# Kernel optimization log

Hardware: AMD Instinct MI355X
Metric: run time of the kernel (lower is better)

The kernel has to match this reference:

```python
import jax, jax.numpy as jnp
import numpy as np

NUM_HEADS = 16


def setup_inputs() -> dict:
    key = jax.random.key(0)
    ks = jax.random.split(key, 5)
    B, S, D = 2, 2048, 1024
    scale = 0.02
    return {
        "x": jax.random.normal(ks[0], (B, S, D), dtype=jnp.float32),
        "Wq": jax.random.normal(ks[1], (D, D), dtype=jnp.float32) * scale,
        "Wk": jax.random.normal(ks[2], (D, D), dtype=jnp.float32) * scale,
        "Wv": jax.random.normal(ks[3], (D, D), dtype=jnp.float32) * scale,
        "Wo": jax.random.normal(ks[4], (D, D), dtype=jnp.float32) * scale,
        "bo": jnp.zeros((D,), dtype=jnp.float32),
    }


def reference(x, Wq, Wk, Wv, Wo, bo):
    B, S, D = x.shape
    H = NUM_HEADS
    Dh = D // H
    # project and split heads -> [B, H, S, Dh]
    q = (x @ Wq).reshape(B, S, H, Dh).transpose(0, 2, 1, 3)
    k = (x @ Wk).reshape(B, S, H, Dh).transpose(0, 2, 1, 3)
    v = (x @ Wv).reshape(B, S, H, Dh).transpose(0, 2, 1, 3)
    # full causal attention scores [B, H, S, S]
    scores = jnp.einsum("bhqd,bhkd->bhqk", q, k)
    causal_mask = jnp.triu(jnp.ones((S, S), dtype=bool), k=1)
    scores = jnp.where(causal_mask, -jnp.inf, scores)
    attn = jax.nn.softmax(scores / jnp.sqrt(jnp.float32(Dh)), axis=-1)
    ctx = jnp.einsum("bhqk,bhkd->bhqd", attn, v)
    ctx = ctx.transpose(0, 2, 1, 3).reshape(B, S, D)
    return ctx @ Wo + bo
```

## Files before the change

kernel.cpp:

```cpp
#include <hip/hip_runtime.h>
#include <hip/hip_bf16.h>
#include <math.h>

typedef __bf16 bf16_t;
typedef bf16_t bf16x4 __attribute__((ext_vector_type(4)));
typedef bf16_t bf16x8 __attribute__((ext_vector_type(8)));
typedef float f32x4 __attribute__((ext_vector_type(4)));

#define MFMA16(a, b, c) __builtin_amdgcn_mfma_f32_16x16x32_bf16(a, b, c, 0, 0, 0)
#define NEG_BIG (-1e30f)
#define QSCALE 0.18033688f

#define GLL16(gp, lp)                                                          \
    __builtin_amdgcn_global_load_lds(                                          \
        (const __attribute__((address_space(1))) unsigned int*)(gp),           \
        (__attribute__((address_space(3))) unsigned int*)(lp), 16, 0, 0)


__global__ __launch_bounds__(256) void prep(const float* __restrict__ x,
                                            const float* __restrict__ Wq,
                                            const float* __restrict__ Wk,
                                            const float* __restrict__ Wv,
                                            const float* __restrict__ Wo,
                                            bf16_t* __restrict__ Xb,
                                            bf16_t* __restrict__ WTqkv,
                                            bf16_t* __restrict__ WoT) {
    __shared__ float tile[32][33];
    const int z = blockIdx.z;
    const int tx = threadIdx.x, ty = threadIdx.y;
    if (z == 4) {
        int i0 = (((blockIdx.y * 32 + blockIdx.x) * 256) + ty * 32 + tx) * 4;
        for (int j = 0; j < 4; j++) {
            int i = i0 + j * 1048576;
            float4 v = *(const float4*)(x + i);
            Xb[i + 0] = (bf16_t)v.x;
            Xb[i + 1] = (bf16_t)v.y;
            Xb[i + 2] = (bf16_t)v.z;
            Xb[i + 3] = (bf16_t)v.w;
        }
    } else {
        const float* W = (z == 0) ? Wq : (z == 1) ? Wk : (z == 2) ? Wv : Wo;
        bf16_t* WT = (z < 3) ? (WTqkv + (size_t)z * 1048576) : WoT;
        int bx = blockIdx.x * 32, by = blockIdx.y * 32;
        for (int i = 0; i < 32; i += 8)
            tile[ty + i][tx] = W[(size_t)(by + ty + i) * 1024 + bx + tx];
        __syncthreads();
        for (int i = 0; i < 32; i += 8)
            WT[(size_t)(bx + ty + i) * 1024 + by + tx] = (bf16_t)tile[tx][ty + i];
    }
}

__global__ __launch_bounds__(256) void gemm_qkv(const bf16_t* __restrict__ X,
                                                const bf16_t* __restrict__ WT,
                                                bf16_t* __restrict__ Qd,
                                                bf16_t* __restrict__ Kd,
                                                bf16_t* __restrict__ Vd) {
    __shared__ bf16_t AsmF[128 * 64];
    __shared__ bf16_t BsmF[128 * 64];
    const int which = blockIdx.z;
    const bf16_t* Wt = WT + (size_t)which * 1024 * 1024;
    const int bm = blockIdx.y * 128;
    const int bn = blockIdx.x * 128;
    const int tid = threadIdx.x;
    const int wave = tid >> 6, lane = tid & 63;
    const int wm = (wave >> 1) * 64, wn = (wave & 1) * 64;
    const int col = lane & 15, quad = lane >> 4;
    const int cswz = col & 7;
    const int lr8 = lane >> 3;
    const int jg = (lane & 7) ^ lr8;

    const int srow = wave * 32 + lr8;
    const bf16_t* gA = X  + (size_t)(bm + srow) * 1024 + jg * 8;
    const bf16_t* gB = Wt + (size_t)(bn + srow) * 1024 + jg * 8;
    bf16_t* lA = AsmF + wave * 2048;
    bf16_t* lB = BsmF + wave * 2048;

    f32x4 acc[4][4] = {};

    for (int k0 = 0; k0 < 1024; k0 += 64) {
        for (int j = 0; j < 4; j++) {
            GLL16(gA + (size_t)j * 8192 + k0, lA + j * 512);
            GLL16(gB + (size_t)j * 8192 + k0, lB + j * 512);
        }
        __syncthreads();
        for (int ks = 0; ks < 2; ks++) {
            bf16x8 af[4], bfr[4];
            for (int mi = 0; mi < 4; mi++)
                af[mi] = *(const bf16x8*)&AsmF[(wm + mi * 16 + col) * 64 +
                                               (((ks << 2) + quad) ^ cswz) * 8];
            for (int ni = 0; ni < 4; ni++)
                bfr[ni] = *(const bf16x8*)&BsmF[(wn + ni * 16 + col) * 64 +
                                                (((ks << 2) + quad) ^ cswz) * 8];
            if (which != 2) {
                for (int mi = 0; mi < 4; mi++)
                    for (int ni = 0; ni < 4; ni++)
                        acc[mi][ni] = MFMA16(af[mi], bfr[ni], acc[mi][ni]);
            } else {
                for (int mi = 0; mi < 4; mi++)
                    for (int ni = 0; ni < 4; ni++)
                        acc[mi][ni] = MFMA16(bfr[ni], af[mi], acc[mi][ni]);
            }
        }
        __syncthreads();
    }

    if (which != 2) {
        const float sc = (which == 0) ? QSCALE : 1.0f;
        for (int mi = 0; mi < 4; mi++) {
            for (int ni = 0; ni < 4; ni++) {
                int mbase = bm + wm + mi * 16 + quad * 4;
                int n = bn + wn + ni * 16 + col;
                int h = n >> 6, dh = n & 63;
                for (int r = 0; r < 4; r++) {
                    int m = mbase + r;
                    int b = m >> 11, s = m & 2047;
                    size_t bh = (size_t)b * 16 + h;
                    bf16_t val = (bf16_t)(acc[mi][ni][r] * sc);
                    if (which == 0) Qd[(bh * 2048 + s) * 64 + dh] = val;
                    else            Kd[(bh * 2048 + s) * 64 + dh] = val;
                }
            }
        }
    } else {
        for (int mi = 0; mi < 4; mi++) {
            for (int ni = 0; ni < 4; ni++) {
                int nbase = bn + wn + ni * 16 + quad * 4;
                int m = bm + wm + mi * 16 + col;
                int b = m >> 11, s = m & 2047;
                for (int r = 0; r < 4; r++) {
                    int n = nbase + r;
                    int h = n >> 6, dh = n & 63;
                    size_t bh = (size_t)b * 16 + h;
                    Vd[(bh * 64 + dh) * 2048 + s] = (bf16_t)acc[mi][ni][r];
                }
            }
        }
    }
}

#define PSD 72
__global__ __launch_bounds__(256) void attn(const bf16_t* __restrict__ Q,
                                            const bf16_t* __restrict__ K,
                                            const bf16_t* __restrict__ VT,
                                            bf16_t* __restrict__ CTX) {
    __shared__ bf16_t KsF[2 * 64 * 64];
    __shared__ bf16_t VsF[2 * 64 * 64];
    __shared__ bf16_t Ps[4][16][PSD];

    const int bidx = blockIdx.x;
    const int bh = bidx & 31;
    const int pr = bidx >> 5;
    const int qt0 = pr, qt1 = 31 - pr;
    const int tid = threadIdx.x;
    const int wave = tid >> 6, lane = tid & 63;
    const int col = lane & 15, quad = lane >> 4;
    const int cswz = col & 7;
    const int lr8 = lane >> 3;
    const int jg = (lane & 7) ^ lr8;

    const bf16_t* Qb = Q + (size_t)bh * 2048 * 64;
    const bf16_t* Kb = K + (size_t)bh * 2048 * 64;
    const bf16_t* Vb = VT + (size_t)bh * 64 * 2048;

    const int strow = wave * 16 + lr8;
    const bf16_t* gK = Kb + (size_t)strow * 64 + jg * 8;
    const bf16_t* gV = Vb + (size_t)strow * 2048 + jg * 8;

    const int b_ = bh >> 4, h_ = bh & 15;

    bf16x8 ones;
    for (int i = 0; i < 8; i++) ones[i] = (bf16_t)1.0f;

    auto stage = [&](int k0, int bsel) {
        bf16_t* lK = KsF + bsel * 4096 + wave * 1024;
        bf16_t* lV = VsF + bsel * 4096 + wave * 1024;
        for (int j = 0; j < 2; j++) {
            GLL16(gK + (size_t)(k0 + j * 8) * 64, lK + j * 512);
            GLL16(gV + (size_t)(k0 + j * 8 * 2048), lV + j * 512);
        }
    };

    stage(0, 0);

    int q0 = qt0 * 64;
    int qrow = q0 + wave * 16 + col;
    bf16x8 qf0 = *(const bf16x8*)&Qb[(size_t)qrow * 64 + quad * 8];
    bf16x8 qf1 = *(const bf16x8*)&Qb[(size_t)qrow * 64 + 32 + quad * 8];

    f32x4 o[4] = {};
    f32x4 accl = {};

    for (int g = 0; g < 33; g++) {
        __syncthreads();
        if (g < 32) {
            int gn = g + 1;
            int k0n = (gn <= qt0 ? gn : gn - qt0 - 1) * 64;
            stage(k0n, gn & 1);
        }

        const int bsel = g & 1;
        const bf16_t* Kbuf = KsF + bsel * 4096;
        const bf16_t* Vbuf = VsF + bsel * 4096;
        const bool diag = (g == qt0) || (g == 32);

        for (int ksub = 0; ksub < 4; ksub++) {
            bf16x8 a0 = *(const bf16x8*)&Kbuf[(ksub * 16 + col) * 64 +
                                              (quad ^ cswz) * 8];
            bf16x8 a1 = *(const bf16x8*)&Kbuf[(ksub * 16 + col) * 64 +
                                              ((4 + quad) ^ cswz) * 8];
            f32x4 z = {};
            z = MFMA16(a0, qf0, z);
            z = MFMA16(a1, qf1, z);
            if (diag) {
                for (int r = 0; r < 4; r++) {
                    int lk = ksub * 16 + quad * 4 + r;
                    if (lk > wave * 16 + col) z[r] = NEG_BIG;
                }
            }
            bf16x4 pw;
            for (int r = 0; r < 4; r++)
                pw[r] = (bf16_t)exp2f(z[r]);
            *(bf16x4*)&Ps[wave][col][ksub * 16 + quad * 4] = pw;
        }

        for (int ck = 0; ck < 2; ck++) {
            bf16x8 pf = *(const bf16x8*)&Ps[wave][col][ck * 32 + quad * 8];
            accl = MFMA16(pf, ones, accl);
            for (int d = 0; d < 4; d++) {
                bf16x8 vf = *(const bf16x8*)&Vbuf[(d * 16 + col) * 64 +
                                                  (((ck << 2) + quad) ^ cswz) * 8];
                o[d] = MFMA16(pf, vf, o[d]);
            }
        }

        if (g == qt0) {
            for (int d = 0; d < 4; d++) {
                for (int r = 0; r < 4; r++) {
                    int s = q0 + wave * 16 + quad * 4 + r;
                    CTX[((size_t)(b_ * 2048 + s)) * 1024 + h_ * 64 + d * 16 + col] =
                        (bf16_t)(o[d][r] / fmaxf(accl[r], 1e-20f));
                }
                o[d] = f32x4{};
            }
            accl = f32x4{};
            q0 = qt1 * 64;
            qrow = q0 + wave * 16 + col;
            qf0 = *(const bf16x8*)&Qb[(size_t)qrow * 64 + quad * 8];
            qf1 = *(const bf16x8*)&Qb[(size_t)qrow * 64 + 32 + quad * 8];
        }
    }

    for (int d = 0; d < 4; d++) {
        for (int r = 0; r < 4; r++) {
            int s = q0 + wave * 16 + quad * 4 + r;
            CTX[((size_t)(b_ * 2048 + s)) * 1024 + h_ * 64 + d * 16 + col] =
                (bf16_t)(o[d][r] / fmaxf(accl[r], 1e-20f));
        }
    }
}

__global__ __launch_bounds__(256) void gemm_out(const bf16_t* __restrict__ X,
                                                const bf16_t* __restrict__ WT,
                                                const float* __restrict__ BO,
                                                float* __restrict__ OUT) {
    __shared__ bf16_t AsmF[64 * 64];
    __shared__ bf16_t BsmF[128 * 64];
    const int bm = blockIdx.y * 64;
    const int bn = blockIdx.x * 128;
    const int tid = threadIdx.x;
    const int wave = tid >> 6, lane = tid & 63;
    const int wm = (wave >> 1) * 32, wn = (wave & 1) * 64;
    const int col = lane & 15, quad = lane >> 4;
    const int cswz = col & 7;
    const int lr8 = lane >> 3;
    const int jg = (lane & 7) ^ lr8;

    const int arow = wave * 16 + lr8;
    const int brow = wave * 32 + lr8;
    const bf16_t* gA = X  + (size_t)(bm + arow) * 1024 + jg * 8;
    const bf16_t* gB = WT + (size_t)(bn + brow) * 1024 + jg * 8;
    bf16_t* lA = AsmF + wave * 1024;
    bf16_t* lB = BsmF + wave * 2048;

    f32x4 acc[2][4] = {};

    for (int k0 = 0; k0 < 1024; k0 += 64) {
        for (int j = 0; j < 2; j++)
            GLL16(gA + (size_t)j * 8192 + k0, lA + j * 512);
        for (int j = 0; j < 4; j++)
            GLL16(gB + (size_t)j * 8192 + k0, lB + j * 512);
        __syncthreads();
        for (int ks = 0; ks < 2; ks++) {
            bf16x8 af[2], bfr[4];
            for (int mi = 0; mi < 2; mi++)
                af[mi] = *(const bf16x8*)&AsmF[(wm + mi * 16 + col) * 64 +
                                               (((ks << 2) + quad) ^ cswz) * 8];
            for (int ni = 0; ni < 4; ni++)
                bfr[ni] = *(const bf16x8*)&BsmF[(wn + ni * 16 + col) * 64 +
                                                (((ks << 2) + quad) ^ cswz) * 8];
            for (int mi = 0; mi < 2; mi++)
                for (int ni = 0; ni < 4; ni++)
                    acc[mi][ni] = MFMA16(af[mi], bfr[ni], acc[mi][ni]);
        }
        __syncthreads();
    }

    for (int mi = 0; mi < 2; mi++) {
        for (int ni = 0; ni < 4; ni++) {
            int mbase = bm + wm + mi * 16 + quad * 4;
            int n = bn + wn + ni * 16 + col;
            float bov = BO[n];
            for (int r = 0; r < 4; r++) {
                int m = mbase + r;
                OUT[(size_t)m * 1024 + n] = acc[mi][ni][r] + bov;
            }
        }
    }
}

extern "C" void kernel_launch(void* const* d_in, const int* in_sizes, int n_in,
                              void* d_out, int out_size, void* d_ws, size_t ws_size,
                              hipStream_t stream) {
    const float* x  = (const float*)d_in[0];
    const float* Wq = (const float*)d_in[1];
    const float* Wk = (const float*)d_in[2];
    const float* Wv = (const float*)d_in[3];
    const float* Wo = (const float*)d_in[4];
    const float* bo = (const float*)d_in[5];
    float* out = (float*)d_out;

    const size_t MEG = 1048576;
    bf16_t* base  = (bf16_t*)d_ws;
    bf16_t* Xb    = base;
    bf16_t* WTqkv = base + 4 * MEG;
    bf16_t* WoT   = base + 7 * MEG;
    bf16_t* Qb    = base + 8 * MEG;
    bf16_t* Kb    = base + 12 * MEG;
    bf16_t* Vb    = base + 16 * MEG;
    bf16_t* Cb    = base + 20 * MEG;

    prep<<<dim3(32, 32, 5), dim3(32, 8), 0, stream>>>(x, Wq, Wk, Wv, Wo,
                                                      Xb, WTqkv, WoT);
    gemm_qkv<<<dim3(8, 32, 3), 256, 0, stream>>>(Xb, WTqkv, Qb, Kb, Vb);
    attn<<<512, 256, 0, stream>>>(Qb, Kb, Vb, Cb);
    gemm_out<<<dim3(8, 64), 256, 0, stream>>>(Cb, WoT, bo, out);
}
```

Before: 189.8 us.

## Give each attention block one query tile instead of a paired tile

The attention kernel previously paired query tile pr with tile 31-pr in one block, walking 33 KV tiles so every block did equal work. Now each block handles a single query tile, launching 1024 blocks, with the heaviest tiles scheduled first via reversed indexing. The aim is more parallelism and simpler control flow with no mid-loop epilogue. In exchange, per-block work becomes imbalanced and the grid relies on the hardware scheduler to backfill short blocks.

```diff
diff --git a/kernel.cpp b/kernel.cpp
--- a/kernel.cpp
+++ b/kernel.cpp
@@ -149,8 +149,7 @@
 
     const int bidx = blockIdx.x;
     const int bh = bidx & 31;
-    const int pr = bidx >> 5;
-    const int qt0 = pr, qt1 = 31 - pr;
+    const int qt = 31 - (bidx >> 5);
     const int tid = threadIdx.x;
     const int wave = tid >> 6, lane = tid & 63;
     const int col = lane & 15, quad = lane >> 4;
@@ -182,26 +181,23 @@
 
     stage(0, 0);
 
-    int q0 = qt0 * 64;
-    int qrow = q0 + wave * 16 + col;
-    bf16x8 qf0 = *(const bf16x8*)&Qb[(size_t)qrow * 64 + quad * 8];
-    bf16x8 qf1 = *(const bf16x8*)&Qb[(size_t)qrow * 64 + 32 + quad * 8];
+    const int q0 = qt * 64;
+    const int qrow = q0 + wave * 16 + col;
+    const bf16x8 qf0 = *(const bf16x8*)&Qb[(size_t)qrow * 64 + quad * 8];
+    const bf16x8 qf1 = *(const bf16x8*)&Qb[(size_t)qrow * 64 + 32 + quad * 8];
 
     f32x4 o[4] = {};
     f32x4 accl = {};
 
-    for (int g = 0; g < 33; g++) {
-        __syncthreads();
-        if (g < 32) {
-            int gn = g + 1;
-            int k0n = (gn <= qt0 ? gn : gn - qt0 - 1) * 64;
-            stage(k0n, gn & 1);
-        }
+    const int nt = qt + 1;
+    for (int g = 0; g < nt; g++) {
+        __syncthreads();
+        if (g + 1 < nt) stage((g + 1) * 64, (g + 1) & 1);
 
         const int bsel = g & 1;
         const bf16_t* Kbuf = KsF + bsel * 4096;
         const bf16_t* Vbuf = VsF + bsel * 4096;
-        const bool diag = (g == qt0) || (g == 32);
+        const bool diag = (g == qt);
 
         for (int ksub = 0; ksub < 4; ksub++) {
             bf16x8 a0 = *(const bf16x8*)&Kbuf[(ksub * 16 + col) * 64 +
@@ -231,22 +227,6 @@
                                                   (((ck << 2) + quad) ^ cswz) * 8];
                 o[d] = MFMA16(pf, vf, o[d]);
             }
-        }
-
-        if (g == qt0) {
-            for (int d = 0; d < 4; d++) {
-                for (int r = 0; r < 4; r++) {
-                    int s = q0 + wave * 16 + quad * 4 + r;
-                    CTX[((size_t)(b_ * 2048 + s)) * 1024 + h_ * 64 + d * 16 + col] =
-                        (bf16_t)(o[d][r] / fmaxf(accl[r], 1e-20f));
-                }
-                o[d] = f32x4{};
-            }
-            accl = f32x4{};
-            q0 = qt1 * 64;
-            qrow = q0 + wave * 16 + col;
-            qf0 = *(const bf16x8*)&Qb[(size_t)qrow * 64 + quad * 8];
-            qf1 = *(const bf16x8*)&Qb[(size_t)qrow * 64 + 32 + quad * 8];
         }
     }
 
@@ -342,6 +322,6 @@
     prep<<<dim3(32, 32, 5), dim3(32, 8), 0, stream>>>(x, Wq, Wk, Wv, Wo,
                                                       Xb, WTqkv, WoT);
     gemm_qkv<<<dim3(8, 32, 3), 256, 0, stream>>>(Xb, WTqkv, Qb, Kb, Vb);
-    attn<<<512, 256, 0, stream>>>(Qb, Kb, Vb, Cb);
+    attn<<<1024, 256, 0, stream>>>(Qb, Kb, Vb, Cb);
     gemm_out<<<dim3(8, 64), 256, 0, stream>>>(Cb, WoT, bo, out);
 }
```

Measured after the change: 180.1 us. 5.1% less time.
